# Kernel optimization log

Hardware: AMD Instinct MI355X
Metric: run time of the kernel (lower is better)

The kernel has to match this reference:

```python
import jax, jax.numpy as jnp
import numpy as np

NUM_USERS = 100000
NUM_ITEMS = 50000
EMB_DIM = 128
N_EDGES = 1600000
BATCH = 16384
L_USER = (0, 1, 2)


def setup_inputs() -> dict:
    key = jax.random.key(0)
    k1, k2, k3, k4, k5, k6 = jax.random.split(key, 6)
    users = jax.random.randint(k1, (BATCH,), 0, NUM_USERS)
    items = jax.random.randint(k2, (BATCH,), 0, NUM_ITEMS)
    edge_src = jax.random.randint(k3, (N_EDGES,), 0, NUM_USERS)
    edge_dst = jax.random.randint(k4, (N_EDGES,), 0, NUM_USERS)
    # nn.Parameter init: normal(mean=0, std=0.01)
    user_emb = jax.random.normal(k5, (NUM_USERS, EMB_DIM), dtype=jnp.float32) * 0.01
    item_emb = jax.random.normal(k6, (NUM_ITEMS, EMB_DIM), dtype=jnp.float32) * 0.01
    return {"users": users, "items": items, "edge_src": edge_src,
            "edge_dst": edge_dst, "user_emb": user_emb, "item_emb": item_emb}


def social_conv(edge_src, edge_dst, h):
    # DGL copy_u -> mean aggregation over social (user-user) edges
    msgs = h[edge_src]  # [E, D] gather
    agg = jax.ops.segment_sum(msgs, edge_dst, num_segments=NUM_USERS)  # [N, D]
    deg = jax.ops.segment_sum(jnp.ones_like(edge_dst, dtype=h.dtype), edge_dst,
                              num_segments=NUM_USERS)  # [N]
    return agg / jnp.maximum(deg, 1.0)[:, None]


def reference(users, items, edge_src, edge_dst, user_emb, item_emb):
    g1 = social_conv(edge_src, edge_dst, user_emb)
    g2 = social_conv(edge_src, edge_dst, g1)
    final_user = jnp.zeros_like(user_emb)
    if 0 in L_USER:
        final_user = final_user + user_emb
    if 1 in L_USER:
        final_user = final_user + g1
    if 2 in L_USER:
        final_user = final_user + g2
    latest_user = final_user[users]   # [B, D]
    latest_item = item_emb[items]     # [B, D]
    predict = jax.nn.sigmoid(jnp.sum(latest_user * latest_item, axis=1))  # [B]
    return predict, latest_user, latest_item
```

## Files before the change

### kernel.cpp

```cpp
#include <hip/hip_runtime.h>
#include <math.h>

#define NUM_USERS 100000
#define NUM_ITEMS 50000
#define EMB_D 128
#define N_EDGES 1600000
#define BATCH 16384

#define NBINS 782
#define BIN_CAP 2560
#define CHUNK 4096
#define NCHUNKS 391
#define CAP 64

#define CVT_BLOCKS 3125

#define FP8_SCALE 512.0f
#define FP8_INV   (1.0f / 512.0f)

typedef unsigned int u32;
typedef float f32x2 __attribute__((ext_vector_type(2)));

__global__ void prep_kernel(const float* __restrict__ in, u32* __restrict__ outp,
                            const int* __restrict__ edge_src, const int* __restrict__ edge_dst,
                            int* __restrict__ bin_cnt, u32* __restrict__ coarse) {
    __shared__ int hist[NBINS];
    __shared__ int base[NBINS];
    __shared__ int cnt2[NBINS];
    int blk = blockIdx.x;
    int tid = threadIdx.x;
    if (blk >= NCHUNKS) {
        long long bbase = (long long)(blk - NCHUNKS) * 1024;
        #pragma unroll
        for (int g = 0; g < 4; g++) {
            long long i = bbase + g * 256 + tid;
            float4 a = ((const float4*)in)[i];
            int r = __builtin_amdgcn_cvt_pk_fp8_f32(a.x * FP8_SCALE, a.y * FP8_SCALE, 0, false);
            r = __builtin_amdgcn_cvt_pk_fp8_f32(a.z * FP8_SCALE, a.w * FP8_SCALE, r, true);
            outp[i] = (u32)r;
        }
        return;
    }
    long long c0 = (long long)blk * CHUNK;
    int n = (int)min((long long)CHUNK, (long long)N_EDGES - c0);
    for (int i = tid; i < NBINS; i += 256) { hist[i] = 0; cnt2[i] = 0; }
    __syncthreads();
    for (int i = tid; i < n; i += 256) {
        atomicAdd(&hist[edge_dst[c0 + i] >> 7], 1);
    }
    __syncthreads();
    for (int i = tid; i < NBINS; i += 256) {
        int h = hist[i];
        if (h) base[i] = atomicAdd(&bin_cnt[i], h);
    }
    __syncthreads();
    for (int i = tid; i < n; i += 256) {
        int d = edge_dst[c0 + i];
        int s = edge_src[c0 + i];
        int b = d >> 7;
        int idx = atomicAdd(&cnt2[b], 1);
        int pl = base[b] + idx;
        if (pl >= 0 && pl < BIN_CAP)
            coarse[(long long)b * BIN_CAP + pl] = ((u32)s << 7) | (u32)(d & 127);
    }
}

__global__ void scat_kernel(const int* __restrict__ bin_cnt, const u32* __restrict__ coarse,
                            int* __restrict__ srt, int* __restrict__ counts) {
    __shared__ int cur[128];
    int b = blockIdx.x;
    int tid = threadIdx.x;
    if (tid < 128) cur[tid] = 0;
    __syncthreads();
    int e = min(bin_cnt[b], BIN_CAP);
    long long s = (long long)b * BIN_CAP;
    int binBase = b << 7;
    for (int i = tid; i < e; i += 256) {
        u32 p = coarse[s + i];
        int dl = (int)(p & 127u);
        int pos = atomicAdd(&cur[dl], 1);
        if (pos < CAP)
            srt[(long long)(binBase + dl) * CAP + pos] = (int)(p >> 7);
    }
    __syncthreads();
    if (tid < 128) {
        int u = binBase + tid;
        if (u < NUM_USERS) counts[u] = cur[tid];
    }
}

__global__ void agg_kernel(const int* __restrict__ counts, const int* __restrict__ srt,
                           const u32* __restrict__ tab32, u32* __restrict__ out32) {
    int wid = (blockIdx.x * blockDim.x + threadIdx.x) >> 6;
    int lane = threadIdx.x & 63;
    if (wid >= NUM_USERS) return;
    wid = __builtin_amdgcn_readfirstlane(wid);
    int cnt = counts[wid];
    int cl = min(cnt, CAP);
    long long start = (long long)wid * CAP;
    int dlane = lane & 31;
    int hi = lane >> 5;
    float4 acc = make_float4(0.f, 0.f, 0.f, 0.f);
    int j = 0;
    for (; j + 16 <= cl; j += 16) {
        int rr[8];
        #pragma unroll
        for (int k = 0; k < 8; k++) {
            int s0 = srt[start + j + 2 * k];
            int s1 = srt[start + j + 2 * k + 1];
            rr[k] = hi ? s1 : s0;
        }
        u32 pp[8];
        #pragma unroll
        for (int k = 0; k < 8; k++) pp[k] = tab32[(long long)rr[k] * 32 + dlane];
        #pragma unroll
        for (int k = 0; k < 8; k++) {
            f32x2 d0 = __builtin_amdgcn_cvt_pk_f32_fp8((int)pp[k], false);
            f32x2 d1 = __builtin_amdgcn_cvt_pk_f32_fp8((int)pp[k], true);
            acc.x += d0.x; acc.y += d0.y; acc.z += d1.x; acc.w += d1.y;
        }
    }
    if (j < cl) {
        int rr[8]; float ww[8];
        #pragma unroll
        for (int k = 0; k < 8; k++) {
            int i0 = min(j + 2 * k, cl - 1);
            int i1 = min(j + 2 * k + 1, cl - 1);
            int s0 = srt[start + i0];
            int s1 = srt[start + i1];
            rr[k] = hi ? s1 : s0;
            ww[k] = ((j + 2 * k + hi) < cl) ? 1.0f : 0.0f;
        }
        u32 pp[8];
        #pragma unroll
        for (int k = 0; k < 8; k++) pp[k] = tab32[(long long)rr[k] * 32 + dlane];
        #pragma unroll
        for (int k = 0; k < 8; k++) {
            f32x2 d0 = __builtin_amdgcn_cvt_pk_f32_fp8((int)pp[k], false);
            f32x2 d1 = __builtin_amdgcn_cvt_pk_f32_fp8((int)pp[k], true);
            acc.x += d0.x * ww[k]; acc.y += d0.y * ww[k];
            acc.z += d1.x * ww[k]; acc.w += d1.y * ww[k];
        }
    }
    acc.x += __shfl_xor(acc.x, 32, 64);
    acc.y += __shfl_xor(acc.y, 32, 64);
    acc.z += __shfl_xor(acc.z, 32, 64);
    acc.w += __shfl_xor(acc.w, 32, 64);
    float inv = 1.0f / fmaxf((float)cnt, 1.0f);
    int enc = __builtin_amdgcn_cvt_pk_fp8_f32(acc.x * inv, acc.y * inv, 0, false);
    enc = __builtin_amdgcn_cvt_pk_fp8_f32(acc.z * inv, acc.w * inv, enc, true);
    if (lane < 32) out32[(long long)wid * 32 + dlane] = (u32)enc;
}

__global__ void final_kernel(const int* __restrict__ users, const int* __restrict__ items,
                             const float* __restrict__ user_emb, const float* __restrict__ item_emb,
                             const u32* __restrict__ g18, const int* __restrict__ counts,
                             const int* __restrict__ srt,
                             float* __restrict__ out_predict, float* __restrict__ out_lu,
                             float* __restrict__ out_li) {
    int b = (blockIdx.x * blockDim.x + threadIdx.x) >> 6;
    int lane = threadIdx.x & 63;
    if (b >= BATCH) return;
    b = __builtin_amdgcn_readfirstlane(b);
    int u = users[b];
    int it = items[b];
    int cnt = counts[u];
    int cl = min(cnt, CAP);
    long long start = (long long)u * CAP;
    int dlane = lane & 31;
    int hi = lane >> 5;
    float4 acc = make_float4(0.f, 0.f, 0.f, 0.f);
    int j = 0;
    for (; j + 16 <= cl; j += 16) {
        int rr[8];
        #pragma unroll
        for (int k = 0; k < 8; k++) {
            int s0 = srt[start + j + 2 * k];
            int s1 = srt[start + j + 2 * k + 1];
            rr[k] = hi ? s1 : s0;
        }
        u32 pp[8];
        #pragma unroll
        for (int k = 0; k < 8; k++) pp[k] = g18[(long long)rr[k] * 32 + dlane];
        #pragma unroll
        for (int k = 0; k < 8; k++) {
            f32x2 d0 = __builtin_amdgcn_cvt_pk_f32_fp8((int)pp[k], false);
            f32x2 d1 = __builtin_amdgcn_cvt_pk_f32_fp8((int)pp[k], true);
            acc.x += d0.x; acc.y += d0.y; acc.z += d1.x; acc.w += d1.y;
        }
    }
    if (j < cl) {
        int rr[8]; float ww[8];
        #pragma unroll
        for (int k = 0; k < 8; k++) {
            int i0 = min(j + 2 * k, cl - 1);
            int i1 = min(j + 2 * k + 1, cl - 1);
            int s0 = srt[start + i0];
            int s1 = srt[start + i1];
            rr[k] = hi ? s1 : s0;
            ww[k] = ((j + 2 * k + hi) < cl) ? 1.0f : 0.0f;
        }
        u32 pp[8];
        #pragma unroll
        for (int k = 0; k < 8; k++) pp[k] = g18[(long long)rr[k] * 32 + dlane];
        #pragma unroll
        for (int k = 0; k < 8; k++) {
            f32x2 d0 = __builtin_amdgcn_cvt_pk_f32_fp8((int)pp[k], false);
            f32x2 d1 = __builtin_amdgcn_cvt_pk_f32_fp8((int)pp[k], true);
            acc.x += d0.x * ww[k]; acc.y += d0.y * ww[k];
            acc.z += d1.x * ww[k]; acc.w += d1.y * ww[k];
        }
    }
    acc.x += __shfl_xor(acc.x, 32, 64);
    acc.y += __shfl_xor(acc.y, 32, 64);
    acc.z += __shfl_xor(acc.z, 32, 64);
    acc.w += __shfl_xor(acc.w, 32, 64);
    float inv = (1.0f / fmaxf((float)cnt, 1.0f)) * FP8_INV;
    float4 ue = *(const float4*)(user_emb + (long long)u * EMB_D + dlane * 4);
    u32 a1p = g18[(long long)u * 32 + dlane];
    f32x2 a0 = __builtin_amdgcn_cvt_pk_f32_fp8((int)a1p, false);
    f32x2 a1 = __builtin_amdgcn_cvt_pk_f32_fp8((int)a1p, true);
    float4 ie = *(const float4*)(item_emb + (long long)it * EMB_D + dlane * 4);
    float4 lu;
    lu.x = ue.x + a0.x * FP8_INV + acc.x * inv;
    lu.y = ue.y + a0.y * FP8_INV + acc.y * inv;
    lu.z = ue.z + a1.x * FP8_INV + acc.z * inv;
    lu.w = ue.w + a1.y * FP8_INV + acc.w * inv;
    if (lane < 32) {
        *(float4*)(out_lu + (long long)b * EMB_D + dlane * 4) = lu;
        *(float4*)(out_li + (long long)b * EMB_D + dlane * 4) = ie;
    }
    float dot = lu.x * ie.x + lu.y * ie.y + lu.z * ie.z + lu.w * ie.w;
    #pragma unroll
    for (int off = 16; off > 0; off >>= 1) dot += __shfl_down(dot, off, 64);
    if (lane == 0) out_predict[b] = 1.0f / (1.0f + expf(-dot));
}

extern "C" void kernel_launch(void* const* d_in, const int* in_sizes, int n_in,
                              void* d_out, int out_size, void* d_ws, size_t ws_size,
                              hipStream_t stream) {
    const int* users     = (const int*)d_in[0];
    const int* items     = (const int*)d_in[1];
    const int* edge_src  = (const int*)d_in[2];
    const int* edge_dst  = (const int*)d_in[3];
    const float* user_emb = (const float*)d_in[4];
    const float* item_emb = (const float*)d_in[5];

    int* ws_i = (int*)d_ws;
    int* bin_cnt = ws_i;
    int* counts  = bin_cnt + 1024;
    int* srt     = counts + 100352;
    u32* coarse  = (u32*)(srt + (long long)NUM_USERS * CAP);
    u32* ue8     = coarse + (long long)NBINS * BIN_CAP;
    u32* g18     = ue8 + 3200000;

    float* out_predict = (float*)d_out;
    float* out_lu = out_predict + BATCH;
    float* out_li = out_lu + (long long)BATCH * EMB_D;

    hipMemsetAsync(bin_cnt, 0, 1024 * sizeof(int), stream);

    prep_kernel<<<NCHUNKS + CVT_BLOCKS, 256, 0, stream>>>(
        user_emb, ue8, edge_src, edge_dst, bin_cnt, coarse);

    scat_kernel<<<NBINS, 256, 0, stream>>>(bin_cnt, coarse, srt, counts);

    agg_kernel<<<(NUM_USERS + 3) / 4, 256, 0, stream>>>(counts, srt, ue8, g18);

    final_kernel<<<(BATCH + 3) / 4, 256, 0, stream>>>(
        users, items, user_emb, item_emb, g18, counts, srt,
        out_predict, out_lu, out_li);
}
```

Measured before the change: 226.7 us.

## Replace global bin atomics with per-chunk fixed cells and LDS-staged scatter

The edge binning pass no longer does a histogram pass plus global atomic reservation. Each chunk (now twice as large) writes directly into its own fixed-size cell per bin and records a byte count, which removes the memset and the global atomics. The scatter kernel then walks every cell slot for its bin, builds the per-user CAP-sized lists in shared memory, and writes them out with coalesced int4 stores. The cost is a much larger coarse buffer (every bin×chunk cell is read, including empty slots) and possible edge loss if a cell overflows its 40-entry capacity. The coarse buffer is aliased with g18, since it is dead by the time g18 is written.

After: 232.4 us. 2.5% more time.

```diff
diff --git a/kernel.cpp b/kernel.cpp
--- a/kernel.cpp
+++ b/kernel.cpp
@@ -8,9 +8,9 @@
 #define BATCH 16384
 
 #define NBINS 782
-#define BIN_CAP 2560
-#define CHUNK 4096
-#define NCHUNKS 391
+#define CHUNK 8192
+#define NCHUNKS 196
+#define CELL 40
 #define CAP 64
 
 #define CVT_BLOCKS 3125
@@ -19,13 +19,12 @@
 #define FP8_INV   (1.0f / 512.0f)
 
 typedef unsigned int u32;
+typedef unsigned char u8;
 typedef float f32x2 __attribute__((ext_vector_type(2)));
 
 __global__ void prep_kernel(const float* __restrict__ in, u32* __restrict__ outp,
                             const int* __restrict__ edge_src, const int* __restrict__ edge_dst,
-                            int* __restrict__ bin_cnt, u32* __restrict__ coarse) {
-    __shared__ int hist[NBINS];
-    __shared__ int base[NBINS];
+                            u32* __restrict__ coarse, u8* __restrict__ cellcnt) {
     __shared__ int cnt2[NBINS];
     int blk = blockIdx.x;
     int tid = threadIdx.x;
@@ -43,50 +42,58 @@
     }
     long long c0 = (long long)blk * CHUNK;
     int n = (int)min((long long)CHUNK, (long long)N_EDGES - c0);
-    for (int i = tid; i < NBINS; i += 256) { hist[i] = 0; cnt2[i] = 0; }
-    __syncthreads();
-    for (int i = tid; i < n; i += 256) {
-        atomicAdd(&hist[edge_dst[c0 + i] >> 7], 1);
-    }
-    __syncthreads();
-    for (int i = tid; i < NBINS; i += 256) {
-        int h = hist[i];
-        if (h) base[i] = atomicAdd(&bin_cnt[i], h);
-    }
-    __syncthreads();
-    for (int i = tid; i < n; i += 256) {
-        int d = edge_dst[c0 + i];
-        int s = edge_src[c0 + i];
-        int b = d >> 7;
-        int idx = atomicAdd(&cnt2[b], 1);
-        int pl = base[b] + idx;
-        if (pl >= 0 && pl < BIN_CAP)
-            coarse[(long long)b * BIN_CAP + pl] = ((u32)s << 7) | (u32)(d & 127);
-    }
-}
-
-__global__ void scat_kernel(const int* __restrict__ bin_cnt, const u32* __restrict__ coarse,
+    for (int i = tid; i < NBINS; i += 256) cnt2[i] = 0;
+    __syncthreads();
+    int n4 = n >> 2;
+    const int4* d4p = (const int4*)(edge_dst + c0);
+    const int4* s4p = (const int4*)(edge_src + c0);
+    for (int i = tid; i < n4; i += 256) {
+        int4 d = d4p[i];
+        int4 s = s4p[i];
+        int dd[4] = {d.x, d.y, d.z, d.w};
+        int ss[4] = {s.x, s.y, s.z, s.w};
+        #pragma unroll
+        for (int k = 0; k < 4; k++) {
+            int b = dd[k] >> 7;
+            int idx = atomicAdd(&cnt2[b], 1);
+            if (idx < CELL)
+                coarse[((long long)b * NCHUNKS + blk) * CELL + idx] =
+                    ((u32)ss[k] << 7) | (u32)(dd[k] & 127);
+        }
+    }
+    __syncthreads();
+    for (int i = tid; i < NBINS; i += 256)
+        cellcnt[(long long)blk * NBINS + i] = (u8)min(cnt2[i], CELL);
+}
+
+__global__ void scat_kernel(const u32* __restrict__ coarse, const u8* __restrict__ cellcnt,
                             int* __restrict__ srt, int* __restrict__ counts) {
     __shared__ int cur[128];
+    __shared__ __align__(16) int stage[128 * CAP];
     int b = blockIdx.x;
     int tid = threadIdx.x;
     if (tid < 128) cur[tid] = 0;
     __syncthreads();
-    int e = min(bin_cnt[b], BIN_CAP);
-    long long s = (long long)b * BIN_CAP;
+    long long cb = (long long)b * NCHUNKS * CELL;
+    for (int i = tid; i < NCHUNKS * CELL; i += 256) {
+        int cell = i / CELL;
+        int slot = i - cell * CELL;
+        if (slot < (int)cellcnt[(long long)cell * NBINS + b]) {
+            u32 p = coarse[cb + i];
+            int dl = (int)(p & 127u);
+            int pos = atomicAdd(&cur[dl], 1);
+            if (pos < CAP) stage[(dl << 6) + pos] = (int)(p >> 7);
+        }
+    }
+    __syncthreads();
     int binBase = b << 7;
-    for (int i = tid; i < e; i += 256) {
-        u32 p = coarse[s + i];
-        int dl = (int)(p & 127u);
-        int pos = atomicAdd(&cur[dl], 1);
-        if (pos < CAP)
-            srt[(long long)(binBase + dl) * CAP + pos] = (int)(p >> 7);
-    }
-    __syncthreads();
-    if (tid < 128) {
-        int u = binBase + tid;
-        if (u < NUM_USERS) counts[u] = cur[tid];
-    }
+    int rows = min(128, NUM_USERS - binBase);
+    long long obase = (long long)binBase * CAP;
+    int nI4 = rows << 4;
+    for (int i4 = tid; i4 < nI4; i4 += 256)
+        ((int4*)(srt + obase))[i4] = ((const int4*)stage)[i4];
+    if (tid < 128 && tid < rows)
+        counts[binBase + tid] = cur[tid];
 }
 
 __global__ void agg_kernel(const int* __restrict__ counts, const int* __restrict__ srt,
@@ -246,24 +253,24 @@
     const float* user_emb = (const float*)d_in[4];
     const float* item_emb = (const float*)d_in[5];
 
+    const long long COARSE_U32 = (long long)NBINS * NCHUNKS * CELL;
+
     int* ws_i = (int*)d_ws;
-    int* bin_cnt = ws_i;
-    int* counts  = bin_cnt + 1024;
-    int* srt     = counts + 100352;
-    u32* coarse  = (u32*)(srt + (long long)NUM_USERS * CAP);
-    u32* ue8     = coarse + (long long)NBINS * BIN_CAP;
-    u32* g18     = ue8 + 3200000;
+    int* counts = ws_i;
+    int* srt    = counts + 100352;
+    u32* ue8    = (u32*)(srt + (long long)NUM_USERS * CAP);
+    u32* coarse = ue8 + 3200000;
+    u8*  cellcnt = (u8*)(coarse + COARSE_U32);
+    u32* g18    = coarse;
 
     float* out_predict = (float*)d_out;
     float* out_lu = out_predict + BATCH;
     float* out_li = out_lu + (long long)BATCH * EMB_D;
 
-    hipMemsetAsync(bin_cnt, 0, 1024 * sizeof(int), stream);
-
     prep_kernel<<<NCHUNKS + CVT_BLOCKS, 256, 0, stream>>>(
-        user_emb, ue8, edge_src, edge_dst, bin_cnt, coarse);
-
-    scat_kernel<<<NBINS, 256, 0, stream>>>(bin_cnt, coarse, srt, counts);
+        user_emb, ue8, edge_src, edge_dst, coarse, cellcnt);
+
+    scat_kernel<<<NBINS, 256, 0, stream>>>(coarse, cellcnt, srt, counts);
 
     agg_kernel<<<(NUM_USERS + 3) / 4, 256, 0, stream>>>(counts, srt, ue8, g18);
 
```
